# Optimization experiments

Measured on AMD Instinct MI355X. Metric: run time of the kernel, lower is better.

The kernel has to match this reference:

```python
import jax, jax.numpy as jnp
import numpy as np

B, S, ENC = 64, 2048, 1024          # batch, encoder seq len, encoder feature dim
U, E_DIM, V_SZ = 512, 256, 50000    # dec_units, embedding_dim, vocab_size
IN_DIM = ENC + E_DIM                # LSTM input: [context ; token embedding]


def setup_inputs() -> dict:
    key = jax.random.key(0)
    ks = jax.random.split(key, 16)
    g = lambda k, shp, s=0.02: (jax.random.normal(k, shp, jnp.float32) * s)
    return {
        "x": jax.random.randint(ks[0], (B, 1), 0, V_SZ),
        "c_fwd": g(ks[1], (B, U), 0.1),
        "c_bwd": g(ks[2], (B, U), 0.1),
        "enc_output": jax.random.normal(ks[3], (B, S, ENC), jnp.float32),
        "emb": g(ks[4], (V_SZ, E_DIM)),
        "W1_w": g(ks[5], (ENC, U)), "W1_b": jnp.zeros((U,), jnp.float32),
        "W2_w": g(ks[6], (U, U)),   "W2_b": jnp.zeros((U,), jnp.float32),
        "W3_w": g(ks[7], (U, U)),   "W3_b": jnp.zeros((U,), jnp.float32),
        "V_w": g(ks[8], (U, 1)),    "V_b": jnp.zeros((1,), jnp.float32),
        "Kf": g(ks[9], (IN_DIM, 4 * U)),  "bf": jnp.zeros((4 * U,), jnp.float32),
        "Kb": g(ks[10], (IN_DIM, 4 * U)), "bb": jnp.zeros((4 * U,), jnp.float32),
        "fc_w": g(ks[11], (2 * U, V_SZ)), "fc_b": jnp.zeros((V_SZ,), jnp.float32),
    }


def _lstm_step_zero_state(xin, K, b):
    # Keras LSTM single step from zero (h0, c0): recurrent term vanishes.
    # Gate order in Keras kernel: i, f, c(g), o.
    z = xin @ K + b
    i, f, g, o = jnp.split(z, 4, axis=-1)
    i, o = jax.nn.sigmoid(i), jax.nn.sigmoid(o)  # f gate multiplies c0=0
    c = i * jnp.tanh(g)
    h = o * jnp.tanh(c)
    return h, c


def reference(x, c_fwd, c_bwd, enc_output, emb,
              W1_w, W1_b, W2_w, W2_b, W3_w, W3_b, V_w, V_b,
              Kf, bf, Kb, bb, fc_w, fc_b):
    # Bahdanau additive attention: score [B, S, 1]
    hidden_proj = (c_fwd @ W2_w + W2_b + c_bwd @ W3_w + W3_b)[:, None, :]  # [B,1,U]
    score = jnp.tanh(enc_output @ W1_w + W1_b + hidden_proj) @ V_w + V_b
    attn = jax.nn.softmax(score, axis=1)                 # softmax over S
    ctx = jnp.sum(attn * enc_output, axis=1)             # [B, ENC]

    xe = emb[x[:, 0]]                                    # [B, E_DIM]
    xin = jnp.concatenate([ctx, xe], axis=-1)            # [B, ENC+E_DIM]

    # Bidirectional LSTM over a length-1 sequence from zero initial state:
    # both directions see the same single timestep with separate weights.
    hf, cf = _lstm_step_zero_state(xin, Kf, bf)
    hb, cb = _lstm_step_zero_state(xin, Kb, bb)

    out = jnp.concatenate([hf, hb], axis=-1)             # [B, 2U]
    logits = out @ fc_w + fc_b                           # [B, vocab]
    return logits, hf, cf, hb, cb
```

## Files before the change

### kernel.cpp

```cpp
#include <hip/hip_runtime.h>

using u16 = unsigned short;
typedef float f32x4 __attribute__((ext_vector_type(4)));
typedef float f32x16 __attribute__((ext_vector_type(16)));
typedef __bf16 bf16x8 __attribute__((ext_vector_type(8)));
typedef u16 u16x8 __attribute__((ext_vector_type(8)));
typedef u16 u16x4 __attribute__((ext_vector_type(4)));

static constexpr int OF_HPB   = 262144;
static constexpr int OF_CTXP  = 294912;
static constexpr int OF_STATS = 2392064;
static constexpr int OF_XIN   = 2396160;
static constexpr int OF_ZPART = 2478080;
static constexpr int OF_HHL   = 3002368;
static constexpr size_t SCRATCH_FLOATS = 3067904;
static constexpr size_t SCRATCH_BYTES  = SCRATCH_FLOATS * 4ull;

__device__ __forceinline__ u16 f2bf(float f) {
  unsigned u = __float_as_uint(f);
  u += 0x7FFFu + ((u >> 16) & 1u);
  return (u16)(u >> 16);
}
__device__ __forceinline__ float bf2f(u16 u) {
  return __uint_as_float((unsigned)u << 16);
}
__device__ __forceinline__ float fast_tanh(float x) {
  x = fminf(fmaxf(x, -20.f), 20.f);
  float e = __expf(2.f * x);
  return (e - 1.f) / (e + 1.f);
}
__device__ __forceinline__ float fast_sig(float x) { return 1.f / (1.f + __expf(-x)); }

__global__ void k_prep_w1(const float* __restrict__ W1w, u16* __restrict__ w1p) {
  __shared__ float tile[16][516];
  const int t = threadIdx.x;
  const int ks = blockIdx.x;
  {
    int kk = t >> 4, u0 = (t & 15) * 32;
    const float* src = W1w + (size_t)(ks * 16 + kk) * 512 + u0;
    #pragma unroll
    for (int i = 0; i < 8; ++i)
      *(float4*)&tile[kk][u0 + i * 4] = *(const float4*)(src + i * 4);
  }
  __syncthreads();
  #pragma unroll
  for (int q = 0; q < 4; ++q) {
    int c = t + q * 256;
    int wv = c >> 6, l = c & 63;
    int u = wv * 32 + (l & 31), koct = l >> 5;
    u16x8 p;
    #pragma unroll
    for (int e = 0; e < 8; ++e) p[e] = f2bf(tile[koct * 8 + e][u]);
    *(u16x8*)(w1p + (size_t)ks * 8192 + (size_t)c * 8) = p;
  }
}

__global__ void k_prep_hp(const float* __restrict__ cf, const float* __restrict__ cb,
                          const float* __restrict__ W2w, const float* __restrict__ W2b,
                          const float* __restrict__ W3w, const float* __restrict__ W3b,
                          const float* __restrict__ W1b, float* __restrict__ hpb) {
  __shared__ float cfl[512], cbl[512];
  const int b = blockIdx.x, t = threadIdx.x;
  cfl[t] = cf[(size_t)b * 512 + t];       cfl[t + 256] = cf[(size_t)b * 512 + t + 256];
  cbl[t] = cb[(size_t)b * 512 + t];       cbl[t + 256] = cb[(size_t)b * 512 + t + 256];
  __syncthreads();
  const int u1 = t, u2 = t + 256;
  float a1 = W2b[u1] + W3b[u1] + W1b[u1];
  float a2 = W2b[u2] + W3b[u2] + W1b[u2];
  for (int k = 0; k < 512; ++k) {
    float c1 = cfl[k], c2 = cbl[k];
    const float* r2 = W2w + (size_t)k * 512;
    const float* r3 = W3w + (size_t)k * 512;
    a1 += c1 * r2[u1] + c2 * r3[u1];
    a2 += c1 * r2[u2] + c2 * r3[u2];
  }
  hpb[(size_t)b * 512 + u1] = a1;
  hpb[(size_t)b * 512 + u2] = a2;
}

__global__ void __launch_bounds__(1024, 8)
k_attn(const float* __restrict__ enc, const u16* __restrict__ w1p,
       const float* __restrict__ hpb, const float* __restrict__ Vw,
       const float* __restrict__ Vb, u16* __restrict__ ctxp,
       float* __restrict__ stats) {
  __shared__ __align__(16) u16 As[32768];
  __shared__ float epi[3648];

  const int t = threadIdx.x;
  const int bid = blockIdx.x;
  const int b = bid >> 6, tile = bid & 63;
  const size_t row0 = (size_t)b * 2048 + (size_t)tile * 32;

  const int l = t & 63, wv = t >> 6;

  {
    const int r = t >> 5, cl = t & 31;
    const float* src = enc + (row0 + r) * 1024 + cl * 4;
    #pragma unroll
    for (int i = 0; i < 8; ++i) {
      float4 v = *(const float4*)(src + i * 128);
      const int c0 = i * 128 + cl * 4;
      u16x4 w4;
      w4[0] = f2bf(v.x); w4[1] = f2bf(v.y); w4[2] = f2bf(v.z); w4[3] = f2bf(v.w);
      *(u16x4*)(As + (c0 >> 4) * 512 + (((c0 >> 3) & 1) * 32 + r) * 8 + (c0 & 7)) = w4;
    }
  }
  __syncthreads();

  const u16* bbase = w1p + (size_t)wv * 512 + (size_t)l * 8;
  f32x16 acc;
  #pragma unroll
  for (int i = 0; i < 16; ++i) acc[i] = 0.f;

  bf16x8 b0 = *(const bf16x8*)(bbase);
  bf16x8 b1 = *(const bf16x8*)(bbase + 8192);
  #pragma unroll 4
  for (int ks = 0; ks < 64; ++ks) {
    bf16x8 a = *(const bf16x8*)(As + ks * 512 + l * 8);
    acc = __builtin_amdgcn_mfma_f32_32x32x16_bf16(a, b0, acc, 0, 0, 0);
    b0 = b1;
    if (ks < 62) b1 = *(const bf16x8*)(bbase + (size_t)(ks + 2) * 8192);
  }

  float* red = epi;
  float* scv = epi + 544;
  float* pcv = epi + 576;

  const int ucol = (wv << 5) + (l & 31);
  const float vwv = Vw[ucol];
  const float hpv = hpb[(size_t)b * 512 + ucol];
  const int hi4 = (l >> 5) * 4;
  const bool writer = ((l & 31) == 0);
  #pragma unroll
  for (int r = 0; r < 16; ++r) {
    float s = vwv * fast_tanh(acc[r] + hpv);
    s += __shfl_xor(s, 1);
    s += __shfl_xor(s, 2);
    s += __shfl_xor(s, 4);
    s += __shfl_xor(s, 8);
    s += __shfl_xor(s, 16);
    if (writer) {
      int sl = (r & 3) + 8 * (r >> 2) + hi4;
      red[sl * 17 + wv] = s;
    }
  }
  __syncthreads();
  if (t < 32) {
    float s = Vb[0];
    #pragma unroll
    for (int wq = 0; wq < 16; ++wq) s += red[t * 17 + wq];
    float e = __expf(s);
    scv[t] = e;
    float p = e;
    p += __shfl_xor(p, 1);  p += __shfl_xor(p, 2);  p += __shfl_xor(p, 4);
    p += __shfl_xor(p, 8);  p += __shfl_xor(p, 16);
    if (t == 0) stats[bid] = p;
  }
  __syncthreads();

  {
    const int c4 = (t & 255) * 4;
    const int rq = t >> 8;
    const int ks = c4 >> 4, koct = (c4 >> 3) & 1, e0 = c4 & 7;
    float ax = 0.f, ay = 0.f, az = 0.f, aw2 = 0.f;
    #pragma unroll
    for (int r = 0; r < 8; ++r) {
      const int row = rq * 8 + r;
      u16x4 v = *(const u16x4*)(As + ks * 512 + (koct * 32 + row) * 8 + e0);
      float sc = scv[row];
      ax += sc * bf2f(v[0]); ay += sc * bf2f(v[1]);
      az += sc * bf2f(v[2]); aw2 += sc * bf2f(v[3]);
    }
    if (rq) {
      float4 st = {ax, ay, az, aw2};
      *(float4*)&pcv[(rq - 1) * 1024 + c4] = st;
    }
    __syncthreads();
    if (rq == 0) {
      float4 p1 = *(const float4*)&pcv[c4];
      float4 p2 = *(const float4*)&pcv[1024 + c4];
      float4 p3 = *(const float4*)&pcv[2048 + c4];
      u16x4 o;
      o[0] = f2bf(ax + p1.x + p2.x + p3.x);
      o[1] = f2bf(ay + p1.y + p2.y + p3.y);
      o[2] = f2bf(az + p1.z + p2.z + p3.z);
      o[3] = f2bf(aw2 + p1.w + p2.w + p3.w);
      *(u16x4*)(ctxp + (size_t)bid * 1024 + c4) = o;
    }
  }
}

__global__ void k_attn_reduce(const u16* __restrict__ ctxp, const float* __restrict__ stats,
                              const int* __restrict__ x, const float* __restrict__ emb,
                              float* __restrict__ xin) {
  __shared__ float ps[64];
  __shared__ float invs;
  const int b = blockIdx.x, t = threadIdx.x;
  if (t < 64) ps[t] = stats[b * 64 + t];
  __syncthreads();
  if (t == 0) {
    float s = 0.f;
    #pragma unroll
    for (int i = 0; i < 64; ++i) s += ps[i];
    invs = 1.f / s;
  }
  __syncthreads();
  const float inv = invs;
  {
    const int c4 = t * 4;
    float a0 = 0.f, a1 = 0.f, a2 = 0.f, a3 = 0.f;
    for (int ch = 0; ch < 64; ++ch) {
      u16x4 v = *(const u16x4*)(ctxp + ((size_t)b * 64 + ch) * 1024 + c4);
      a0 += bf2f(v[0]); a1 += bf2f(v[1]); a2 += bf2f(v[2]); a3 += bf2f(v[3]);
    }
    float4 o = {a0 * inv, a1 * inv, a2 * inv, a3 * inv};
    *(float4*)&xin[(size_t)b * 1280 + c4] = o;
  }
  xin[(size_t)b * 1280 + 1024 + t] = emb[(size_t)x[b] * 256 + t];
}

__global__ void k_lstm_gemm(const float* __restrict__ xin, const float* __restrict__ Kf,
                            const float* __restrict__ Kb, float* __restrict__ zpart) {
  __shared__ float xl[32][68];
  const int t = threadIdx.x;
  const int bid = blockIdx.x;
  const int dir = bid >> 7;
  const int jt  = (bid >> 1) & 63;
  const int ks  = bid & 1;
  const float* K = dir ? Kb : Kf;
  const int j  = jt * 32 + (t & 31);
  const int tb = t >> 5;
  const int brow = t >> 2, kq = (t & 3) * 8;
  float acc[8] = {0,0,0,0,0,0,0,0};
  for (int k0 = ks * 640; k0 < ks * 640 + 640; k0 += 32) {
    float4 x0 = *(const float4*)&xin[(size_t)brow * 1280 + k0 + kq];
    float4 x1 = *(const float4*)&xin[(size_t)brow * 1280 + k0 + kq + 4];
    __syncthreads();
    xl[kq+0][brow]=x0.x; xl[kq+1][brow]=x0.y; xl[kq+2][brow]=x0.z; xl[kq+3][brow]=x0.w;
    xl[kq+4][brow]=x1.x; xl[kq+5][brow]=x1.y; xl[kq+6][brow]=x1.z; xl[kq+7][brow]=x1.w;
    __syncthreads();
    const float* Kp = K + (size_t)k0 * 2048 + j;
    #pragma unroll 8
    for (int kk = 0; kk < 32; ++kk) {
      float wv = Kp[(size_t)kk * 2048];
      float4 v0 = *(const float4*)&xl[kk][tb * 8];
      float4 v1 = *(const float4*)&xl[kk][tb * 8 + 4];
      acc[0] += v0.x * wv; acc[1] += v0.y * wv; acc[2] += v0.z * wv; acc[3] += v0.w * wv;
      acc[4] += v1.x * wv; acc[5] += v1.y * wv; acc[6] += v1.z * wv; acc[7] += v1.w * wv;
    }
  }
  float* zp = zpart + ((size_t)dir * 2 + ks) * 64 * 2048;
  #pragma unroll
  for (int i = 0; i < 8; ++i)
    zp[(size_t)(tb * 8 + i) * 2048 + j] = acc[i];
}

__global__ void k_gates(const float* __restrict__ zpart, const float* __restrict__ bfv,
                        const float* __restrict__ bbv, float* __restrict__ dout,
                        u16* __restrict__ hhl) {
  const int dir = blockIdx.x >> 6, b = blockIdx.x & 63, u = threadIdx.x;
  const float* bias = dir ? bbv : bfv;
  const float* z0 = zpart + ((size_t)dir * 2 + 0) * 131072 + (size_t)b * 2048;
  const float* z1 = zpart + ((size_t)dir * 2 + 1) * 131072 + (size_t)b * 2048;
  float zi = z0[u]        + z1[u]        + bias[u];
  float zg = z0[1024 + u] + z1[1024 + u] + bias[1024 + u];
  float zo = z0[1536 + u] + z1[1536 + u] + bias[1536 + u];
  float c = fast_sig(zi) * fast_tanh(zg);
  float h = fast_sig(zo) * fast_tanh(c);
  size_t base = 3200000u + (size_t)dir * 65536u;
  dout[base + (size_t)b * 512 + u] = h;
  dout[base + 32768u + (size_t)b * 512 + u] = c;
  u16 hi = f2bf(h);
  u16 lo = f2bf(h - bf2f(hi));
  hhl[(size_t)b * 1024 + dir * 512 + u] = hi;
  hhl[65536u + (size_t)b * 1024 + dir * 512 + u] = lo;
}

__global__ void __launch_bounds__(256)
k_fc_mfma(const float* __restrict__ fcw, const u16* __restrict__ hhl,
          const float* __restrict__ fcb, float* __restrict__ logits) {
  __shared__ float Bs[2][32 * 136];
  const int t = threadIdx.x;
  const int j0 = blockIdx.x * 128;
  const int l = t & 63, w = t >> 6;
  const int ln = l & 15, lg = l >> 4;
  const int srow = t >> 3, scol = (t & 7) * 16;
  const bool interior = (j0 + 128 <= 50000);

  f32x4 acc[4][2];
  #pragma unroll
  for (int im = 0; im < 4; ++im)
    #pragma unroll
    for (int nf = 0; nf < 2; ++nf) acc[im][nf] = f32x4{0.f, 0.f, 0.f, 0.f};

  float4 pre[4];
  {
    const float* src = fcw + (size_t)srow * 50000 + j0 + scol;
    if (interior) {
      #pragma unroll
      for (int q = 0; q < 4; ++q) pre[q] = *(const float4*)(src + q * 4);
    } else {
      #pragma unroll
      for (int q = 0; q < 4; ++q) {
        int jb = j0 + scol + q * 4;
        pre[q].x = (jb + 0 < 50000) ? src[q*4 + 0] : 0.f;
        pre[q].y = (jb + 1 < 50000) ? src[q*4 + 1] : 0.f;
        pre[q].z = (jb + 2 < 50000) ? src[q*4 + 2] : 0.f;
        pre[q].w = (jb + 3 < 50000) ? src[q*4 + 3] : 0.f;
      }
    }
    #pragma unroll
    for (int q = 0; q < 4; ++q)
      *(float4*)&Bs[0][srow * 136 + scol + q * 4] = pre[q];
  }
  __syncthreads();

  for (int ks = 0; ks < 32; ++ks) {
    const int cur = ks & 1;
    if (ks < 31) {
      const float* src = fcw + (size_t)(ks + 1) * 32 * 50000 + (size_t)srow * 50000 + j0 + scol;
      if (interior) {
        #pragma unroll
        for (int q = 0; q < 4; ++q) pre[q] = *(const float4*)(src + q * 4);
      } else {
        #pragma unroll
        for (int q = 0; q < 4; ++q) {
          int jb = j0 + scol + q * 4;
          pre[q].x = (jb + 0 < 50000) ? src[q*4 + 0] : 0.f;
          pre[q].y = (jb + 1 < 50000) ? src[q*4 + 1] : 0.f;
          pre[q].z = (jb + 2 < 50000) ? src[q*4 + 2] : 0.f;
          pre[q].w = (jb + 3 < 50000) ? src[q*4 + 3] : 0.f;
        }
      }
    }
    bf16x8 ahi[4], alo[4];
    #pragma unroll
    for (int im = 0; im < 4; ++im) {
      const u16* ha = hhl + (size_t)(im * 16 + ln) * 1024 + ks * 32 + lg * 8;
      ahi[im] = *(const bf16x8*)(ha);
      alo[im] = *(const bf16x8*)(ha + 65536);
    }
    bf16x8 bfr[2];
    #pragma unroll
    for (int nf = 0; nf < 2; ++nf) {
      u16x8 pv;
      #pragma unroll
      for (int i = 0; i < 8; ++i)
        pv[i] = f2bf(Bs[cur][(lg * 8 + i) * 136 + w * 32 + nf * 16 + ln]);
      bfr[nf] = *(bf16x8*)&pv;
    }
    #pragma unroll
    for (int im = 0; im < 4; ++im)
      #pragma unroll
      for (int nf = 0; nf < 2; ++nf) {
        acc[im][nf] = __builtin_amdgcn_mfma_f32_16x16x32_bf16(alo[im], bfr[nf], acc[im][nf], 0, 0, 0);
        acc[im][nf] = __builtin_amdgcn_mfma_f32_16x16x32_bf16(ahi[im], bfr[nf], acc[im][nf], 0, 0, 0);
      }
    if (ks < 31) {
      #pragma unroll
      for (int q = 0; q < 4; ++q)
        *(float4*)&Bs[cur ^ 1][srow * 136 + scol + q * 4] = pre[q];
    }
    __syncthreads();
  }

  #pragma unroll
  for (int nf = 0; nf < 2; ++nf) {
    int c = j0 + w * 32 + nf * 16 + ln;
    if (c < 50000) {
      float fb = fcb[c];
      #pragma unroll
      for (int im = 0; im < 4; ++im)
        #pragma unroll
        for (int r = 0; r < 4; ++r) {
          int row = im * 16 + lg * 4 + r;
          logits[(size_t)row * 50000 + c] = acc[im][nf][r] + fb;
        }
    }
  }
}

__global__ void __launch_bounds__(256)
k_fc_f32(const float* __restrict__ dout_ro, const float* __restrict__ fcw,
         const float* __restrict__ fcb, float* __restrict__ logits) {
  __shared__ float ol[64][68];
  __shared__ float wl[64][132];
  const int t = threadIdx.x;
  const int j0 = blockIdx.x * 128;
  const int tb = t >> 5, tj = t & 31;
  const float* hf = dout_ro + 3200000u;
  const float* hb = dout_ro + 3200000u + 65536u;
  float acc[8][4];
  #pragma unroll
  for (int bi = 0; bi < 8; ++bi)
    #pragma unroll
    for (int ji = 0; ji < 4; ++ji) acc[bi][ji] = 0.f;

  for (int k0 = 0; k0 < 1024; k0 += 64) {
    __syncthreads();
    {
      int bb = t >> 2, kq = (t & 3) * 16;
      const float* src = (k0 < 512) ? (hf + (size_t)bb * 512 + k0 + kq)
                                    : (hb + (size_t)bb * 512 + (k0 - 512) + kq);
      #pragma unroll
      for (int i = 0; i < 4; ++i) {
        float4 v = *(const float4*)(src + i * 4);
        ol[kq + i*4 + 0][bb] = v.x;
        ol[kq + i*4 + 1][bb] = v.y;
        ol[kq + i*4 + 2][bb] = v.z;
        ol[kq + i*4 + 3][bb] = v.w;
      }
    }
    {
      int kk = t >> 2, jh = (t & 3) * 32;
      const float* wsrc = fcw + (size_t)(k0 + kk) * 50000 + j0 + jh;
      #pragma unroll
      for (int i = 0; i < 8; ++i) {
        int j = j0 + jh + i * 4;
        float4 v;
        if (j + 3 < 50000) {
          v = *(const float4*)(wsrc + i * 4);
        } else {
          v.x = (j + 0 < 50000) ? wsrc[i*4 + 0] : 0.f;
          v.y = (j + 1 < 50000) ? wsrc[i*4 + 1] : 0.f;
          v.z = (j + 2 < 50000) ? wsrc[i*4 + 2] : 0.f;
          v.w = 0.f;
        }
        *(float4*)&wl[kk][jh + i * 4] = v;
      }
    }
    __syncthreads();
    #pragma unroll 4
    for (int kk = 0; kk < 64; ++kk) {
      float4 wv = *(const float4*)&wl[kk][tj * 4];
      float4 q0 = *(const float4*)&ol[kk][tb * 8];
      float4 q1 = *(const float4*)&ol[kk][tb * 8 + 4];
      float obv[8] = {q0.x, q0.y, q0.z, q0.w, q1.x, q1.y, q1.z, q1.w};
      #pragma unroll
      for (int bi = 0; bi < 8; ++bi) {
        acc[bi][0] += obv[bi] * wv.x;
        acc[bi][1] += obv[bi] * wv.y;
        acc[bi][2] += obv[bi] * wv.z;
        acc[bi][3] += obv[bi] * wv.w;
      }
    }
  }

  const int j = j0 + tj * 4;
  if (j + 3 < 50000) {
    float4 fb = *(const float4*)(fcb + j);
    #pragma unroll
    for (int bi = 0; bi < 8; ++bi) {
      float4 r;
      r.x = acc[bi][0] + fb.x; r.y = acc[bi][1] + fb.y;
      r.z = acc[bi][2] + fb.z; r.w = acc[bi][3] + fb.w;
      *(float4*)&logits[(size_t)(tb * 8 + bi) * 50000 + j] = r;
    }
  } else {
    for (int ji = 0; ji < 4; ++ji) {
      if (j + ji < 50000) {
        float fb = fcb[j + ji];
        for (int bi = 0; bi < 8; ++bi)
          logits[(size_t)(tb * 8 + bi) * 50000 + j + ji] = acc[bi][ji] + fb;
      }
    }
  }
}

extern "C" void kernel_launch(void* const* d_in, const int* in_sizes, int n_in,
                              void* d_out, int out_size, void* d_ws, size_t ws_size,
                              hipStream_t stream) {
  const int*   x    = (const int*)  d_in[0];
  const float* cfwd = (const float*)d_in[1];
  const float* cbwd = (const float*)d_in[2];
  const float* enc  = (const float*)d_in[3];
  const float* emb  = (const float*)d_in[4];
  const float* W1w  = (const float*)d_in[5];
  const float* W1b  = (const float*)d_in[6];
  const float* W2w  = (const float*)d_in[7];
  const float* W2b  = (const float*)d_in[8];
  const float* W3w  = (const float*)d_in[9];
  const float* W3b  = (const float*)d_in[10];
  const float* Vw   = (const float*)d_in[11];
  const float* Vb   = (const float*)d_in[12];
  const float* Kf   = (const float*)d_in[13];
  const float* bfv  = (const float*)d_in[14];
  const float* Kb   = (const float*)d_in[15];
  const float* bbv  = (const float*)d_in[16];
  const float* fcw  = (const float*)d_in[17];
  const float* fcb  = (const float*)d_in[18];
  float* out = (float*)d_out;

  const bool haveWs = (ws_size >= SCRATCH_BYTES);
  float* S = haveWs ? (float*)d_ws : out;
  u16*   w1p   = (u16*)S;
  float* hpb   = S + OF_HPB;
  u16*   ctxp  = (u16*)(S + OF_CTXP);
  float* stats = S + OF_STATS;
  float* xin   = S + OF_XIN;
  float* zpart = S + OF_ZPART;
  u16*   hhl   = (u16*)(S + OF_HHL);

  k_prep_w1<<<64, 256, 0, stream>>>(W1w, w1p);
  k_prep_hp<<<64, 256, 0, stream>>>(cfwd, cbwd, W2w, W2b, W3w, W3b, W1b, hpb);
  k_attn<<<4096, 1024, 0, stream>>>(enc, w1p, hpb, Vw, Vb, ctxp, stats);
  k_attn_reduce<<<64, 256, 0, stream>>>(ctxp, stats, x, emb, xin);
  k_lstm_gemm<<<256, 256, 0, stream>>>(xin, Kf, Kb, zpart);
  k_gates<<<128, 512, 0, stream>>>(zpart, bfv, bbv, out, hhl);
  if (haveWs) k_fc_mfma<<<392, 256, 0, stream>>>(fcw, hhl, fcb, out);
  else        k_fc_f32<<<391, 256, 0, stream>>>(out, fcw, fcb, out);
}
```

Baseline: 544.4 us.

## Retile attention GEMM to 128-row blocks with double-buffered K-chunk pipeline

The attention score GEMM now gives each block 128 encoder rows instead of 32, and each wave computes a 4x2 grid of 32x32 MFMA tiles so W1 fragments are reused across four row tiles. Encoder data is staged into a double-buffered 16 KB LDS region in 64-column chunks, with the global loads for chunk k+2 and the bf16 conversion for chunk k+1 overlapped with MFMA on chunk k. Because the LDS no longer holds the whole row tile, the weighted context sum re-reads the fp32 encoder rows from global memory. This costs a second pass over enc in exchange for a quarter of the W1 traffic and far fewer partial context rows to reduce afterwards.

```diff
diff --git a/kernel.cpp b/kernel.cpp
--- a/kernel.cpp
+++ b/kernel.cpp
@@ -9,11 +9,11 @@
 
 static constexpr int OF_HPB   = 262144;
 static constexpr int OF_CTXP  = 294912;
-static constexpr int OF_STATS = 2392064;
-static constexpr int OF_XIN   = 2396160;
-static constexpr int OF_ZPART = 2478080;
-static constexpr int OF_HHL   = 3002368;
-static constexpr size_t SCRATCH_FLOATS = 3067904;
+static constexpr int OF_STATS = 819200;
+static constexpr int OF_XIN   = 820224;
+static constexpr int OF_ZPART = 902144;
+static constexpr int OF_HHL   = 1426432;
+static constexpr size_t SCRATCH_FLOATS = 1491968;
 static constexpr size_t SCRATCH_BYTES  = SCRATCH_FLOATS * 4ull;
 
 __device__ __forceinline__ u16 f2bf(float f) {
@@ -46,8 +46,8 @@
   #pragma unroll
   for (int q = 0; q < 4; ++q) {
     int c = t + q * 256;
-    int wv = c >> 6, l = c & 63;
-    int u = wv * 32 + (l & 31), koct = l >> 5;
+    int ug = c >> 6, l = c & 63;
+    int u = ug * 32 + (l & 31), koct = l >> 5;
     u16x8 p;
     #pragma unroll
     for (int e = 0; e < 8; ++e) p[e] = f2bf(tile[koct * 8 + e][u]);
@@ -78,114 +78,164 @@
   hpb[(size_t)b * 512 + u2] = a2;
 }
 
-__global__ void __launch_bounds__(1024, 8)
+__global__ void __launch_bounds__(512, 2)
 k_attn(const float* __restrict__ enc, const u16* __restrict__ w1p,
        const float* __restrict__ hpb, const float* __restrict__ Vw,
        const float* __restrict__ Vb, u16* __restrict__ ctxp,
        float* __restrict__ stats) {
-  __shared__ __align__(16) u16 As[32768];
-  __shared__ float epi[3648];
+  __shared__ __align__(16) u16 smem[16384];
 
   const int t = threadIdx.x;
   const int bid = blockIdx.x;
-  const int b = bid >> 6, tile = bid & 63;
-  const size_t row0 = (size_t)b * 2048 + (size_t)tile * 32;
+  const int b = bid >> 4, tile = bid & 15;
+  const size_t row0 = (size_t)b * 2048 + (size_t)tile * 128;
 
   const int l = t & 63, wv = t >> 6;
 
+  const int srow = t >> 2, skq = (t & 3) * 16;
+  const int smi = srow >> 5, srl = srow & 31, sksl = t & 3;
+  const float* sbase = enc + (row0 + srow) * 1024 + skq;
+  const int sdo = sksl * 2048 + smi * 512 + srl * 8;
+
+  f32x16 acc[4][2];
+  #pragma unroll
+  for (int mi = 0; mi < 4; ++mi)
+    #pragma unroll
+    for (int ni = 0; ni < 2; ++ni)
+      #pragma unroll
+      for (int i = 0; i < 16; ++i) acc[mi][ni][i] = 0.f;
+
+  float4 sr0, sr1, sr2, sr3;
   {
-    const int r = t >> 5, cl = t & 31;
-    const float* src = enc + (row0 + r) * 1024 + cl * 4;
-    #pragma unroll
-    for (int i = 0; i < 8; ++i) {
-      float4 v = *(const float4*)(src + i * 128);
-      const int c0 = i * 128 + cl * 4;
-      u16x4 w4;
-      w4[0] = f2bf(v.x); w4[1] = f2bf(v.y); w4[2] = f2bf(v.z); w4[3] = f2bf(v.w);
-      *(u16x4*)(As + (c0 >> 4) * 512 + (((c0 >> 3) & 1) * 32 + r) * 8 + (c0 & 7)) = w4;
-    }
-  }
-  __syncthreads();
-
-  const u16* bbase = w1p + (size_t)wv * 512 + (size_t)l * 8;
-  f32x16 acc;
-  #pragma unroll
-  for (int i = 0; i < 16; ++i) acc[i] = 0.f;
-
-  bf16x8 b0 = *(const bf16x8*)(bbase);
-  bf16x8 b1 = *(const bf16x8*)(bbase + 8192);
-  #pragma unroll 4
-  for (int ks = 0; ks < 64; ++ks) {
-    bf16x8 a = *(const bf16x8*)(As + ks * 512 + l * 8);
-    acc = __builtin_amdgcn_mfma_f32_32x32x16_bf16(a, b0, acc, 0, 0, 0);
-    b0 = b1;
-    if (ks < 62) b1 = *(const bf16x8*)(bbase + (size_t)(ks + 2) * 8192);
-  }
-
+    sr0 = *(const float4*)(sbase);      sr1 = *(const float4*)(sbase + 4);
+    sr2 = *(const float4*)(sbase + 8);  sr3 = *(const float4*)(sbase + 12);
+    u16x8 p0, p1;
+    p0[0]=f2bf(sr0.x); p0[1]=f2bf(sr0.y); p0[2]=f2bf(sr0.z); p0[3]=f2bf(sr0.w);
+    p0[4]=f2bf(sr1.x); p0[5]=f2bf(sr1.y); p0[6]=f2bf(sr1.z); p0[7]=f2bf(sr1.w);
+    p1[0]=f2bf(sr2.x); p1[1]=f2bf(sr2.y); p1[2]=f2bf(sr2.z); p1[3]=f2bf(sr2.w);
+    p1[4]=f2bf(sr3.x); p1[5]=f2bf(sr3.y); p1[6]=f2bf(sr3.z); p1[7]=f2bf(sr3.w);
+    *(u16x8*)(smem + sdo) = p0;
+    *(u16x8*)(smem + sdo + 256) = p1;
+    sr0 = *(const float4*)(sbase + 64);  sr1 = *(const float4*)(sbase + 68);
+    sr2 = *(const float4*)(sbase + 72);  sr3 = *(const float4*)(sbase + 76);
+  }
+  __syncthreads();
+
+  for (int ck = 0; ck < 16; ++ck) {
+    const int cur = ck & 1;
+    if (ck < 15) {
+      u16x8 p0, p1;
+      p0[0]=f2bf(sr0.x); p0[1]=f2bf(sr0.y); p0[2]=f2bf(sr0.z); p0[3]=f2bf(sr0.w);
+      p0[4]=f2bf(sr1.x); p0[5]=f2bf(sr1.y); p0[6]=f2bf(sr1.z); p0[7]=f2bf(sr1.w);
+      p1[0]=f2bf(sr2.x); p1[1]=f2bf(sr2.y); p1[2]=f2bf(sr2.z); p1[3]=f2bf(sr2.w);
+      p1[4]=f2bf(sr3.x); p1[5]=f2bf(sr3.y); p1[6]=f2bf(sr3.z); p1[7]=f2bf(sr3.w);
+      u16* d = smem + ((cur ^ 1) << 13) + sdo;
+      *(u16x8*)(d) = p0;
+      *(u16x8*)(d + 256) = p1;
+    }
+    if (ck < 14) {
+      const float* sp = sbase + (ck + 2) * 64;
+      sr0 = *(const float4*)(sp);      sr1 = *(const float4*)(sp + 4);
+      sr2 = *(const float4*)(sp + 8);  sr3 = *(const float4*)(sp + 12);
+    }
+    const u16* Ac = smem + (cur << 13);
+    #pragma unroll
+    for (int ksl = 0; ksl < 4; ++ksl) {
+      bf16x8 a0 = *(const bf16x8*)(Ac + ksl * 2048 + 0 * 512 + l * 8);
+      bf16x8 a1 = *(const bf16x8*)(Ac + ksl * 2048 + 1 * 512 + l * 8);
+      bf16x8 a2 = *(const bf16x8*)(Ac + ksl * 2048 + 2 * 512 + l * 8);
+      bf16x8 a3 = *(const bf16x8*)(Ac + ksl * 2048 + 3 * 512 + l * 8);
+      const u16* bp = w1p + (size_t)(ck * 4 + ksl) * 8192 + (size_t)(wv * 2) * 512 + l * 8;
+      bf16x8 b0 = *(const bf16x8*)(bp);
+      bf16x8 b1 = *(const bf16x8*)(bp + 512);
+      acc[0][0] = __builtin_amdgcn_mfma_f32_32x32x16_bf16(a0, b0, acc[0][0], 0, 0, 0);
+      acc[0][1] = __builtin_amdgcn_mfma_f32_32x32x16_bf16(a0, b1, acc[0][1], 0, 0, 0);
+      acc[1][0] = __builtin_amdgcn_mfma_f32_32x32x16_bf16(a1, b0, acc[1][0], 0, 0, 0);
+      acc[1][1] = __builtin_amdgcn_mfma_f32_32x32x16_bf16(a1, b1, acc[1][1], 0, 0, 0);
+      acc[2][0] = __builtin_amdgcn_mfma_f32_32x32x16_bf16(a2, b0, acc[2][0], 0, 0, 0);
+      acc[2][1] = __builtin_amdgcn_mfma_f32_32x32x16_bf16(a2, b1, acc[2][1], 0, 0, 0);
+      acc[3][0] = __builtin_amdgcn_mfma_f32_32x32x16_bf16(a3, b0, acc[3][0], 0, 0, 0);
+      acc[3][1] = __builtin_amdgcn_mfma_f32_32x32x16_bf16(a3, b1, acc[3][1], 0, 0, 0);
+    }
+    asm volatile("s_waitcnt lgkmcnt(0)" ::: "memory");
+    __builtin_amdgcn_s_barrier();
+    __builtin_amdgcn_sched_barrier(0);
+  }
+
+  float* epi = (float*)smem;
   float* red = epi;
-  float* scv = epi + 544;
-  float* pcv = epi + 576;
-
-  const int ucol = (wv << 5) + (l & 31);
-  const float vwv = Vw[ucol];
-  const float hpv = hpb[(size_t)b * 512 + ucol];
-  const int hi4 = (l >> 5) * 4;
-  const bool writer = ((l & 31) == 0);
-  #pragma unroll
-  for (int r = 0; r < 16; ++r) {
-    float s = vwv * fast_tanh(acc[r] + hpv);
-    s += __shfl_xor(s, 1);
-    s += __shfl_xor(s, 2);
-    s += __shfl_xor(s, 4);
-    s += __shfl_xor(s, 8);
-    s += __shfl_xor(s, 16);
-    if (writer) {
-      int sl = (r & 3) + 8 * (r >> 2) + hi4;
-      red[sl * 17 + wv] = s;
-    }
-  }
-  __syncthreads();
-  if (t < 32) {
+  float* scv = epi + 1152;
+  float* ps2 = epi + 1280;
+  float* pcv = epi + 1536;
+
+  {
+    const int lu = l & 31;
+    const float vw0 = Vw[wv * 64 + lu];
+    const float vw1 = Vw[wv * 64 + 32 + lu];
+    const float hp0 = hpb[(size_t)b * 512 + wv * 64 + lu];
+    const float hp1 = hpb[(size_t)b * 512 + wv * 64 + 32 + lu];
+    const int hi4 = (l >> 5) * 4;
+    const bool writer = (lu == 0);
+    #pragma unroll
+    for (int mi = 0; mi < 4; ++mi) {
+      #pragma unroll
+      for (int r = 0; r < 16; ++r) {
+        float s = vw0 * fast_tanh(acc[mi][0][r] + hp0)
+                + vw1 * fast_tanh(acc[mi][1][r] + hp1);
+        s += __shfl_xor(s, 1);
+        s += __shfl_xor(s, 2);
+        s += __shfl_xor(s, 4);
+        s += __shfl_xor(s, 8);
+        s += __shfl_xor(s, 16);
+        if (writer) {
+          int row = mi * 32 + (r & 3) + 8 * (r >> 2) + hi4;
+          red[row * 9 + wv] = s;
+        }
+      }
+    }
+  }
+  __syncthreads();
+  if (t < 128) {
     float s = Vb[0];
     #pragma unroll
-    for (int wq = 0; wq < 16; ++wq) s += red[t * 17 + wq];
+    for (int wq = 0; wq < 8; ++wq) s += red[t * 9 + wq];
     float e = __expf(s);
     scv[t] = e;
     float p = e;
     p += __shfl_xor(p, 1);  p += __shfl_xor(p, 2);  p += __shfl_xor(p, 4);
-    p += __shfl_xor(p, 8);  p += __shfl_xor(p, 16);
-    if (t == 0) stats[bid] = p;
-  }
-  __syncthreads();
+    p += __shfl_xor(p, 8);  p += __shfl_xor(p, 16); p += __shfl_xor(p, 32);
+    if ((t & 63) == 0) ps2[t >> 6] = p;
+  }
+  __syncthreads();
+  if (t == 0) stats[bid] = ps2[0] + ps2[1];
 
   {
-    const int c4 = (t & 255) * 4;
-    const int rq = t >> 8;
-    const int ks = c4 >> 4, koct = (c4 >> 3) & 1, e0 = c4 & 7;
-    float ax = 0.f, ay = 0.f, az = 0.f, aw2 = 0.f;
-    #pragma unroll
-    for (int r = 0; r < 8; ++r) {
-      const int row = rq * 8 + r;
-      u16x4 v = *(const u16x4*)(As + ks * 512 + (koct * 32 + row) * 8 + e0);
-      float sc = scv[row];
-      ax += sc * bf2f(v[0]); ay += sc * bf2f(v[1]);
-      az += sc * bf2f(v[2]); aw2 += sc * bf2f(v[3]);
+    const int c8 = (t & 127) * 8;
+    const int rq = t >> 7;
+    const float* ep = enc + (row0 + rq * 32) * 1024 + c8;
+    float a8[8] = {0.f,0.f,0.f,0.f,0.f,0.f,0.f,0.f};
+    for (int r = 0; r < 32; ++r) {
+      float4 v0 = *(const float4*)(ep + (size_t)r * 1024);
+      float4 v1 = *(const float4*)(ep + (size_t)r * 1024 + 4);
+      float sc = scv[rq * 32 + r];
+      a8[0] += sc * v0.x; a8[1] += sc * v0.y; a8[2] += sc * v0.z; a8[3] += sc * v0.w;
+      a8[4] += sc * v1.x; a8[5] += sc * v1.y; a8[6] += sc * v1.z; a8[7] += sc * v1.w;
     }
     if (rq) {
-      float4 st = {ax, ay, az, aw2};
-      *(float4*)&pcv[(rq - 1) * 1024 + c4] = st;
+      float4 s0 = {a8[0], a8[1], a8[2], a8[3]};
+      float4 s1 = {a8[4], a8[5], a8[6], a8[7]};
+      *(float4*)&pcv[(rq - 1) * 1024 + c8] = s0;
+      *(float4*)&pcv[(rq - 1) * 1024 + c8 + 4] = s1;
     }
     __syncthreads();
     if (rq == 0) {
-      float4 p1 = *(const float4*)&pcv[c4];
-      float4 p2 = *(const float4*)&pcv[1024 + c4];
-      float4 p3 = *(const float4*)&pcv[2048 + c4];
-      u16x4 o;
-      o[0] = f2bf(ax + p1.x + p2.x + p3.x);
-      o[1] = f2bf(ay + p1.y + p2.y + p3.y);
-      o[2] = f2bf(az + p1.z + p2.z + p3.z);
-      o[3] = f2bf(aw2 + p1.w + p2.w + p3.w);
-      *(u16x4*)(ctxp + (size_t)bid * 1024 + c4) = o;
+      u16x8 o;
+      #pragma unroll
+      for (int j = 0; j < 8; ++j) {
+        float v = a8[j] + pcv[c8 + j] + pcv[1024 + c8 + j] + pcv[2048 + c8 + j];
+        o[j] = f2bf(v);
+      }
+      *(u16x8*)(ctxp + (size_t)bid * 1024 + c8) = o;
     }
   }
 }
@@ -193,15 +243,15 @@
 __global__ void k_attn_reduce(const u16* __restrict__ ctxp, const float* __restrict__ stats,
                               const int* __restrict__ x, const float* __restrict__ emb,
                               float* __restrict__ xin) {
-  __shared__ float ps[64];
+  __shared__ float ps[16];
   __shared__ float invs;
   const int b = blockIdx.x, t = threadIdx.x;
-  if (t < 64) ps[t] = stats[b * 64 + t];
+  if (t < 16) ps[t] = stats[b * 16 + t];
   __syncthreads();
   if (t == 0) {
     float s = 0.f;
     #pragma unroll
-    for (int i = 0; i < 64; ++i) s += ps[i];
+    for (int i = 0; i < 16; ++i) s += ps[i];
     invs = 1.f / s;
   }
   __syncthreads();
@@ -209,8 +259,8 @@
   {
     const int c4 = t * 4;
     float a0 = 0.f, a1 = 0.f, a2 = 0.f, a3 = 0.f;
-    for (int ch = 0; ch < 64; ++ch) {
-      u16x4 v = *(const u16x4*)(ctxp + ((size_t)b * 64 + ch) * 1024 + c4);
+    for (int ch = 0; ch < 16; ++ch) {
+      u16x4 v = *(const u16x4*)(ctxp + ((size_t)b * 16 + ch) * 1024 + c4);
       a0 += bf2f(v[0]); a1 += bf2f(v[1]); a2 += bf2f(v[2]); a3 += bf2f(v[3]);
     }
     float4 o = {a0 * inv, a1 * inv, a2 * inv, a3 * inv};
@@ -503,7 +553,7 @@
 
   k_prep_w1<<<64, 256, 0, stream>>>(W1w, w1p);
   k_prep_hp<<<64, 256, 0, stream>>>(cfwd, cbwd, W2w, W2b, W3w, W3b, W1b, hpb);
-  k_attn<<<4096, 1024, 0, stream>>>(enc, w1p, hpb, Vw, Vb, ctxp, stats);
+  k_attn<<<1024, 512, 0, stream>>>(enc, w1p, hpb, Vw, Vb, ctxp, stats);
   k_attn_reduce<<<64, 256, 0, stream>>>(ctxp, stats, x, emb, xin);
   k_lstm_gemm<<<256, 256, 0, stream>>>(xin, Kf, Kb, zpart);
   k_gates<<<128, 512, 0, stream>>>(zpart, bfv, bbv, out, hhl);
```

New measurement: 583.0 us. +7.1%, slower.
